# Kernel optimization log

Measured on AMD Instinct MI355X. Metric: run time of the kernel, lower is better.

## Reference

```python
import jax, jax.numpy as jnp
import numpy as np

TEMP = 0.07  # softmax temperature T


def _l2norm(x, axis=1, eps=1e-12):
    return x / jnp.clip(jnp.linalg.norm(x, axis=axis, keepdims=True), eps, None)


def setup_inputs() -> dict:
    key = jax.random.key(0)
    k1, k2, k3, k4 = jax.random.split(key, 4)
    B, K, D = 256, 8192, 128
    q = jax.random.normal(k1, (B, D), dtype=jnp.float32)
    ba_queue = _l2norm(jax.random.normal(k2, (K, D), dtype=jnp.float32))
    nonba_queue = _l2norm(jax.random.normal(k3, (K, D), dtype=jnp.float32))
    targets = jax.random.randint(k4, (B,), 0, 2, dtype=jnp.int64)
    return {"q": q, "ba_queue": ba_queue, "nonba_queue": nonba_queue, "targets": targets}


def reference(q, ba_queue, nonba_queue, targets):
    K = ba_queue.shape[0]
    # encoder output is L2-normalized; queues are detached buffers
    qn = _l2norm(q, axis=1)
    all_feature = jnp.concatenate([qn, ba_queue, nonba_queue], axis=0)  # [N, D]
    all_label = jnp.concatenate([
        targets.astype(jnp.int32),
        jnp.ones((K,), dtype=jnp.int32),
        jnp.zeros((K,), dtype=jnp.int32),
    ])  # [N]
    N = all_feature.shape[0]

    # [N, N] similarity logits
    sim = jnp.matmul(all_feature, all_feature.T) / TEMP
    logits = sim - jax.lax.stop_gradient(jnp.max(sim, axis=1, keepdims=True))

    # positive mask (same label), excluding self
    mask = (all_label[:, None] == all_label[None, :]).astype(jnp.float32)
    logits_mask = 1.0 - jnp.eye(N, dtype=jnp.float32)
    mask = mask * logits_mask

    exp_logits = jnp.exp(logits) * logits_mask
    log_prob = logits - jnp.log(jnp.sum(exp_logits, axis=1, keepdims=True))
    mean_log_prob_pos = jnp.sum(mask * log_prob, axis=1) / jnp.sum(mask, axis=1)
    return -jnp.mean(mean_log_prob_pos)
```

## Files before the change

kernel.cpp:

```cpp
#include <hip/hip_runtime.h>
#include <hip/hip_bf16.h>
#include <stdint.h>

#define TEMPERATURE 0.07f
#define SC 20.6099312f

constexpr int NQ = 256;
constexpr int KQ = 8192;
constexpr int D  = 128;
constexpr int N  = NQ + 2 * KQ;
constexpr int CS = 26;
constexpr int CS2 = CS * 2;
constexpr int BN = 128;
constexpr int RBM = N / 128;
constexpr int RBF = N / 256;
constexpr int PB = 520;
constexpr int LB = 16;

typedef float f32x16 __attribute__((ext_vector_type(16)));
typedef int   i32x4  __attribute__((ext_vector_type(4)));
typedef int   i32x8  __attribute__((ext_vector_type(8)));

constexpr size_t OFF_F32  = 0;
constexpr size_t OFF_8    = OFF_F32  + (size_t)NQ * D * 4;
constexpr size_t OFF_8S   = OFF_8    + (size_t)N * D;
constexpr size_t OFF_PART = OFF_8S   + (size_t)N * D;
constexpr size_t OFF_LP   = OFF_PART + (size_t)CS2 * N * 4;
constexpr size_t OFF_LP2  = OFF_LP   + (size_t)PB * 256 * 4;
constexpr size_t OFF_BSUM = OFF_LP2  + (size_t)LB * 256 * 4;

#define MFMA8(a, b, c) __builtin_amdgcn_mfma_scale_f32_32x32x64_f8f6f4( \
    (a), (b), (c), 0, 0, 0, 0x7f7f7f7f, 0, 0x7f7f7f7f)

__global__ __launch_bounds__(256) void k_prep(const float* __restrict__ q,
                                              const float* __restrict__ ba,
                                              const float* __restrict__ nb,
                                              const long long* __restrict__ tgt,
                                              float* __restrict__ ff,
                                              unsigned char* __restrict__ fb8,
                                              unsigned char* __restrict__ fb8s,
                                              float* __restrict__ lp) {
    __shared__ float red[4][2][128];
    int wid = threadIdx.x >> 6, lane = threadIdx.x & 63;
    int rbase = blockIdx.x * 32 + wid * 8;
    float s0x = 0.f, s0y = 0.f, s1x = 0.f, s1y = 0.f;
    #pragma unroll
    for (int i = 0; i < 8; ++i) {
        int r = rbase + i;
        const float* src = (r < NQ) ? (q + (size_t)r * D)
                         : (r < NQ + KQ) ? (ba + (size_t)(r - NQ) * D)
                         : (nb + (size_t)(r - NQ - KQ) * D);
        float2 v = *(const float2*)(src + lane * 2);
        float a = v.x, b = v.y;
        int lab;
        if (r < NQ) {
            float ss = a * a + b * b;
            #pragma unroll
            for (int m = 1; m < 64; m <<= 1) ss += __shfl_xor(ss, m);
            float scale = 1.0f / fmaxf(sqrtf(ss), 1e-12f);
            a *= scale; b *= scale;
            lab = (int)tgt[r];
            *(float2*)(ff + (size_t)r * D + lane * 2) = make_float2(a, b);
        } else {
            lab = (r < NQ + KQ) ? 1 : 0;
        }
        int w8  = __builtin_amdgcn_cvt_pk_fp8_f32(a, b, 0, false);
        int w8s = __builtin_amdgcn_cvt_pk_fp8_f32(a * SC, b * SC, 0, false);
        *(unsigned short*)(fb8  + (size_t)r * D + lane * 2) = (unsigned short)w8;
        *(unsigned short*)(fb8s + (size_t)r * D + lane * 2) = (unsigned short)w8s;
        if (lab) { s1x += a; s1y += b; } else { s0x += a; s0y += b; }
    }
    red[wid][0][lane * 2]     = s0x;
    red[wid][0][lane * 2 + 1] = s0y;
    red[wid][1][lane * 2]     = s1x;
    red[wid][1][lane * 2 + 1] = s1y;
    __syncthreads();
    int lab2 = threadIdx.x >> 7, d = threadIdx.x & 127;
    float s = red[0][lab2][d] + red[1][lab2][d] + red[2][lab2][d] + red[3][lab2][d];
    lp[(size_t)blockIdx.x * 256 + lab2 * 128 + d] = s;
}

__global__ __launch_bounds__(256) void k_lsum(const float* __restrict__ lp,
                                              float* __restrict__ lp2) {
    int t = threadIdx.x;
    int b0 = blockIdx.x * 33, b1 = min(b0 + 33, PB);
    float s[4] = {0.f, 0.f, 0.f, 0.f};
    for (int b = b0; b < b1; b += 4) {
        #pragma unroll
        for (int j = 0; j < 4; ++j)
            if (b + j < b1) s[j] += lp[(size_t)(b + j) * 256 + t];
    }
    lp2[(size_t)blockIdx.x * 256 + t] = (s[0] + s[1]) + (s[2] + s[3]);
}

__global__ __launch_bounds__(256, 4) void k_main(const unsigned char* __restrict__ fb8,
                                                 const unsigned char* __restrict__ fb8s,
                                                 float* __restrict__ part) {
    __shared__ __align__(16) unsigned char lds[2][BN * 128];
    const int bid = blockIdx.x;
    const int rb = bid / CS, cs = bid % CS;
    const int tid = threadIdx.x;
    const int lane = tid & 63;
    const int wid  = tid >> 6;
    const int wr = wid >> 1, wc = wid & 1;
    const int l31 = lane & 31, lhi = lane >> 5;
    const int rw = rb * 128 + wr * 64;

    int soff[4];
    #pragma unroll
    for (int i = 0; i < 4; ++i) {
        int flat = i * 256 + tid;
        int line = flat >> 4, p = flat & 15;
        int pl = p ^ (line & 15);
        soff[i] = (2 * line + (pl >> 3)) * 128 + (pl & 7) * 16;
    }

#define STAGE(T, B) { \
    const unsigned char* base_ = fb8 + ((size_t)(cs + (T) * CS)) * (BN * 128); \
    _Pragma("unroll") \
    for (int i_ = 0; i_ < 4; ++i_) \
        __builtin_amdgcn_global_load_lds( \
            (const __attribute__((address_space(1))) unsigned int*)(base_ + soff[i_]), \
            (__attribute__((address_space(3))) unsigned int*)(&lds[B][(i_ * 256 + tid) * 16]), \
            16, 0, 0); }

#define SYNC() { asm volatile("s_waitcnt vmcnt(0)" ::: "memory"); __builtin_amdgcn_s_barrier(); }

    i32x8 rf[2][2];
    #pragma unroll
    for (int rs = 0; rs < 2; ++rs)
        #pragma unroll
        for (int s = 0; s < 2; ++s)
            rf[rs][s] = *(const i32x8*)(fb8s + (size_t)(rw + rs * 32 + l31) * D + s * 64 + lhi * 32);

    f32x16 z16;
    #pragma unroll
    for (int e = 0; e < 16; ++e) z16[e] = 0.f;

    float2 ps2[2] = {{0.f, 0.f}, {0.f, 0.f}};

    STAGE(0, 0) SYNC()

    #pragma unroll 1
    for (int t = 0; t < 5; ++t) {
        if (t + 1 < 5) STAGE(t + 1, (t & 1) ^ 1)
        const unsigned char* buf = &lds[t & 1][0];

        f32x16 acc[2][2];
        __builtin_amdgcn_s_setprio(1);
        #pragma unroll
        for (int s = 0; s < 2; ++s) {
            #pragma unroll
            for (int cc = 0; cc < 2; ++cc) {
                int crow = wc * 64 + cc * 32 + l31;
                int line = crow >> 1;
                int pb = ((crow & 1) << 3) + s * 4 + lhi * 2;
                const unsigned char* lb = buf + line * 256;
                i32x4 lo = *(const i32x4*)(lb + ((pb    ) ^ (line & 15)) * 16);
                i32x4 hi = *(const i32x4*)(lb + ((pb + 1) ^ (line & 15)) * 16);
                i32x8 a = {lo[0], lo[1], lo[2], lo[3], hi[0], hi[1], hi[2], hi[3]};
                acc[cc][0] = MFMA8(a, rf[0][s], (s == 0) ? z16 : acc[cc][0]);
                acc[cc][1] = MFMA8(a, rf[1][s], (s == 0) ? z16 : acc[cc][1]);
            }
        }
        __builtin_amdgcn_s_setprio(0);

        #pragma unroll
        for (int cc = 0; cc < 2; ++cc)
            #pragma unroll
            for (int rs = 0; rs < 2; ++rs) {
                float2 p = {0.f, 0.f};
                #pragma unroll
                for (int g = 0; g < 8; ++g) {
                    p.x += __builtin_amdgcn_exp2f(acc[cc][rs][2 * g]);
                    p.y += __builtin_amdgcn_exp2f(acc[cc][rs][2 * g + 1]);
                }
                ps2[rs].x += p.x; ps2[rs].y += p.y;
            }

        SYNC()
    }

    float rsum[2] = {ps2[0].x + ps2[0].y, ps2[1].x + ps2[1].y};
    rsum[0] += __shfl_xor(rsum[0], 32);
    rsum[1] += __shfl_xor(rsum[1], 32);
    if (lane < 32) {
        float* dst = part + (size_t)(cs * 2 + wc) * N + rw + lane;
        dst[0]  = rsum[0];
        dst[32] = rsum[1];
    }
#undef STAGE
#undef SYNC
}

__global__ __launch_bounds__(256) void k_rowfin(const float* __restrict__ part,
                                                const float* __restrict__ ff,
                                                const float* __restrict__ ba,
                                                const float* __restrict__ nb,
                                                const float* __restrict__ lp2,
                                                const long long* __restrict__ tgt,
                                                float* __restrict__ bsum) {
    __shared__ float sS[256];
    __shared__ float red[256];
    __shared__ int scnt[2];
    {
        float s[4] = {0.f, 0.f, 0.f, 0.f};
        #pragma unroll
        for (int b = 0; b < LB; b += 4) {
            #pragma unroll
            for (int j = 0; j < 4; ++j)
                s[j] += lp2[(size_t)(b + j) * 256 + threadIdx.x];
        }
        sS[threadIdx.x] = (s[0] + s[1]) + (s[2] + s[3]);
        if (threadIdx.x < 64) {
            int c = 0;
            #pragma unroll
            for (int i = 0; i < 4; ++i) c += (int)tgt[threadIdx.x + 64 * i];
            #pragma unroll
            for (int m = 1; m < 64; m <<= 1) c += __shfl_xor(c, m);
            if (threadIdx.x == 0) { scnt[0] = (NQ - c) + KQ; scnt[1] = c + KQ; }
        }
    }
    __syncthreads();
    int r = blockIdx.x * 256 + threadIdx.x;
    float se = 0.f;
    #pragma unroll 4
    for (int c = 0; c < CS2; ++c) se += part[(size_t)c * N + r];
    int lab = (r < NQ) ? (int)tgt[r] : ((r < NQ + KQ) ? 1 : 0);
    const float* fsrc = (r < NQ) ? (ff + (size_t)r * D)
                      : (r < NQ + KQ) ? (ba + (size_t)(r - NQ) * D)
                      : (nb + (size_t)(r - NQ - KQ) * D);
    const float4* frow = (const float4*)fsrc;
    const float4* srow = (const float4*)(sS + lab * 128);
    float dS = 0.f, dd = 0.f;
    #pragma unroll
    for (int i = 0; i < 32; ++i) {
        float4 f = frow[i];
        float4 s = srow[i];
        dS += f.x * s.x + f.y * s.y + f.z * s.z + f.w * s.w;
        int wa  = __builtin_amdgcn_cvt_pk_fp8_f32(f.x, f.y, 0, false);
        int wb  = __builtin_amdgcn_cvt_pk_fp8_f32(f.z, f.w, 0, false);
        int wsa = __builtin_amdgcn_cvt_pk_fp8_f32(f.x * SC, f.y * SC, 0, false);
        int wsb = __builtin_amdgcn_cvt_pk_fp8_f32(f.z * SC, f.w * SC, 0, false);
        dd += __builtin_amdgcn_cvt_f32_fp8(wa, 0) * __builtin_amdgcn_cvt_f32_fp8(wsa, 0)
            + __builtin_amdgcn_cvt_f32_fp8(wa, 1) * __builtin_amdgcn_cvt_f32_fp8(wsa, 1)
            + __builtin_amdgcn_cvt_f32_fp8(wb, 0) * __builtin_amdgcn_cvt_f32_fp8(wsb, 0)
            + __builtin_amdgcn_cvt_f32_fp8(wb, 1) * __builtin_amdgcn_cvt_f32_fp8(wsb, 1);
    }
    se -= __builtin_amdgcn_exp2f(dd);
    float lse = logf(se);
    float P = (float)(scnt[lab] - 1);
    float mlpp = (dS - 1.0f) / (TEMPERATURE * P) - lse;
    red[threadIdx.x] = mlpp;
    __syncthreads();
    for (int s2 = 128; s2 > 0; s2 >>= 1) {
        if (threadIdx.x < s2) red[threadIdx.x] += red[threadIdx.x + s2];
        __syncthreads();
    }
    if (threadIdx.x == 0) bsum[blockIdx.x] = red[0];
}

__global__ __launch_bounds__(64) void k_final(const float* __restrict__ bsum,
                                              float* __restrict__ out) {
    float s = bsum[threadIdx.x];
    if (threadIdx.x == 0) s += bsum[64];
    #pragma unroll
    for (int m = 1; m < 64; m <<= 1) s += __shfl_xor(s, m);
    if (threadIdx.x == 0) out[0] = -s / (float)N;
}

extern "C" void kernel_launch(void* const* d_in, const int* in_sizes, int n_in,
                              void* d_out, int out_size, void* d_ws, size_t ws_size,
                              hipStream_t stream) {
    const float* q       = (const float*)d_in[0];
    const float* ba      = (const float*)d_in[1];
    const float* nb      = (const float*)d_in[2];
    const long long* tgt = (const long long*)d_in[3];
    char* ws = (char*)d_ws;
    float*         ff   = (float*)(ws + OFF_F32);
    unsigned char* fb8  = (unsigned char*)(ws + OFF_8);
    unsigned char* fb8s = (unsigned char*)(ws + OFF_8S);
    float*         part = (float*)(ws + OFF_PART);
    float*         lp   = (float*)(ws + OFF_LP);
    float*         lp2  = (float*)(ws + OFF_LP2);
    float*         bsum = (float*)(ws + OFF_BSUM);

    k_prep  <<<PB,       256, 0, stream>>>(q, ba, nb, tgt, ff, fb8, fb8s, lp);
    k_lsum  <<<LB,       256, 0, stream>>>(lp, lp2);
    k_main  <<<RBM * CS, 256, 0, stream>>>(fb8, fb8s, part);
    k_rowfin<<<RBF,      256, 0, stream>>>(part, ff, ba, nb, lp2, tgt, bsum);
    k_final <<<1,         64, 0, stream>>>(bsum, (float*)d_out);
}
```

Baseline: 82.18 us.

## Fuse all stages into one cooperative persistent kernel with grid syncs

Wraps the five kernels (prep, label sum, fp8 MFMA similarity pass, row finalize, final reduce) as device functions and runs them in one cooperative kernel. The grid is sized to the occupancy limit (at most 4 blocks per CU times 256 CUs), and stages are separated by grid.sync. The aim is to remove the per-kernel launch gaps between stages. In exchange, grid-wide barriers are added, the grid-stride loops may balance work worse than one block per tile, and the fused kernel's register use may be constrained by the shared launch bounds. Falls back to the separate launches if the cooperative launch fails.

```diff
diff --git a/kernel.cpp b/kernel.cpp
--- a/kernel.cpp
+++ b/kernel.cpp
@@ -1,6 +1,9 @@
 #include <hip/hip_runtime.h>
+#include <hip/hip_cooperative_groups.h>
 #include <hip/hip_bf16.h>
 #include <stdint.h>
+
+namespace cg = cooperative_groups;
 
 #define TEMPERATURE 0.07f
 #define SC 20.6099312f
@@ -13,6 +16,7 @@
 constexpr int CS2 = CS * 2;
 constexpr int BN = 128;
 constexpr int RBM = N / 128;
+constexpr int NJOB = RBM * CS;
 constexpr int RBF = N / 256;
 constexpr int PB = 520;
 constexpr int LB = 16;
@@ -32,17 +36,19 @@
 #define MFMA8(a, b, c) __builtin_amdgcn_mfma_scale_f32_32x32x64_f8f6f4( \
     (a), (b), (c), 0, 0, 0, 0x7f7f7f7f, 0, 0x7f7f7f7f)
 
-__global__ __launch_bounds__(256) void k_prep(const float* __restrict__ q,
-                                              const float* __restrict__ ba,
-                                              const float* __restrict__ nb,
-                                              const long long* __restrict__ tgt,
-                                              float* __restrict__ ff,
-                                              unsigned char* __restrict__ fb8,
-                                              unsigned char* __restrict__ fb8s,
-                                              float* __restrict__ lp) {
+
+__device__ __forceinline__ void prep_body(int bb,
+                                          const float* __restrict__ q,
+                                          const float* __restrict__ ba,
+                                          const float* __restrict__ nb,
+                                          const long long* __restrict__ tgt,
+                                          float* __restrict__ ff,
+                                          unsigned char* __restrict__ fb8,
+                                          unsigned char* __restrict__ fb8s,
+                                          float* __restrict__ lp) {
     __shared__ float red[4][2][128];
     int wid = threadIdx.x >> 6, lane = threadIdx.x & 63;
-    int rbase = blockIdx.x * 32 + wid * 8;
+    int rbase = bb * 32 + wid * 8;
     float s0x = 0.f, s0y = 0.f, s1x = 0.f, s1y = 0.f;
     #pragma unroll
     for (int i = 0; i < 8; ++i) {
@@ -77,27 +83,29 @@
     __syncthreads();
     int lab2 = threadIdx.x >> 7, d = threadIdx.x & 127;
     float s = red[0][lab2][d] + red[1][lab2][d] + red[2][lab2][d] + red[3][lab2][d];
-    lp[(size_t)blockIdx.x * 256 + lab2 * 128 + d] = s;
-}
-
-__global__ __launch_bounds__(256) void k_lsum(const float* __restrict__ lp,
-                                              float* __restrict__ lp2) {
+    lp[(size_t)bb * 256 + lab2 * 128 + d] = s;
+    __syncthreads();
+}
+
+__device__ __forceinline__ void lsum_body(int bb,
+                                          const float* __restrict__ lp,
+                                          float* __restrict__ lp2) {
     int t = threadIdx.x;
-    int b0 = blockIdx.x * 33, b1 = min(b0 + 33, PB);
+    int b0 = bb * 33, b1 = (b0 + 33 < PB) ? b0 + 33 : PB;
     float s[4] = {0.f, 0.f, 0.f, 0.f};
     for (int b = b0; b < b1; b += 4) {
         #pragma unroll
         for (int j = 0; j < 4; ++j)
             if (b + j < b1) s[j] += lp[(size_t)(b + j) * 256 + t];
     }
-    lp2[(size_t)blockIdx.x * 256 + t] = (s[0] + s[1]) + (s[2] + s[3]);
-}
-
-__global__ __launch_bounds__(256, 4) void k_main(const unsigned char* __restrict__ fb8,
-                                                 const unsigned char* __restrict__ fb8s,
-                                                 float* __restrict__ part) {
+    lp2[(size_t)bb * 256 + t] = (s[0] + s[1]) + (s[2] + s[3]);
+}
+
+__device__ __forceinline__ void main_body(int bid,
+                                          const unsigned char* __restrict__ fb8,
+                                          const unsigned char* __restrict__ fb8s,
+                                          float* __restrict__ part) {
     __shared__ __align__(16) unsigned char lds[2][BN * 128];
-    const int bid = blockIdx.x;
     const int rb = bid / CS, cs = bid % CS;
     const int tid = threadIdx.x;
     const int lane = tid & 63;
@@ -193,13 +201,14 @@
 #undef SYNC
 }
 
-__global__ __launch_bounds__(256) void k_rowfin(const float* __restrict__ part,
-                                                const float* __restrict__ ff,
-                                                const float* __restrict__ ba,
-                                                const float* __restrict__ nb,
-                                                const float* __restrict__ lp2,
-                                                const long long* __restrict__ tgt,
-                                                float* __restrict__ bsum) {
+__device__ __forceinline__ void rowfin_body(int bb,
+                                            const float* __restrict__ part,
+                                            const float* __restrict__ ff,
+                                            const float* __restrict__ ba,
+                                            const float* __restrict__ nb,
+                                            const float* __restrict__ lp2,
+                                            const long long* __restrict__ tgt,
+                                            float* __restrict__ bsum) {
     __shared__ float sS[256];
     __shared__ float red[256];
     __shared__ int scnt[2];
@@ -222,7 +231,7 @@
         }
     }
     __syncthreads();
-    int r = blockIdx.x * 256 + threadIdx.x;
+    int r = bb * 256 + threadIdx.x;
     float se = 0.f;
     #pragma unroll 4
     for (int c = 0; c < CS2; ++c) se += part[(size_t)c * N + r];
@@ -257,25 +266,74 @@
         if (threadIdx.x < s2) red[threadIdx.x] += red[threadIdx.x + s2];
         __syncthreads();
     }
-    if (threadIdx.x == 0) bsum[blockIdx.x] = red[0];
-}
-
-__global__ __launch_bounds__(64) void k_final(const float* __restrict__ bsum,
-                                              float* __restrict__ out) {
-    float s = bsum[threadIdx.x];
-    if (threadIdx.x == 0) s += bsum[64];
-    #pragma unroll
-    for (int m = 1; m < 64; m <<= 1) s += __shfl_xor(s, m);
-    if (threadIdx.x == 0) out[0] = -s / (float)N;
+    if (threadIdx.x == 0) bsum[bb] = red[0];
+    __syncthreads();
+}
+
+__device__ __forceinline__ void final_body(const float* __restrict__ bsum,
+                                           float* __restrict__ out) {
+    if (threadIdx.x < 64) {
+        float s = bsum[threadIdx.x];
+        if (threadIdx.x == 0) s += bsum[64];
+        #pragma unroll
+        for (int m = 1; m < 64; m <<= 1) s += __shfl_xor(s, m);
+        if (threadIdx.x == 0) out[0] = -s / (float)N;
+    }
+}
+
+__global__ __launch_bounds__(256, 4) void k_mega(const float* q, const float* ba,
+                                                 const float* nb, const long long* tgt,
+                                                 float* ff, unsigned char* fb8,
+                                                 unsigned char* fb8s, float* lp,
+                                                 float* lp2, float* part,
+                                                 float* bsum, float* out) {
+    cg::grid_group grid = cg::this_grid();
+    for (int b = blockIdx.x; b < PB; b += gridDim.x)
+        prep_body(b, q, ba, nb, tgt, ff, fb8, fb8s, lp);
+    grid.sync();
+    for (int b = blockIdx.x; b < LB; b += gridDim.x)
+        lsum_body(b, lp, lp2);
+    grid.sync();
+    for (int j = blockIdx.x; j < NJOB; j += gridDim.x)
+        main_body(j, fb8, fb8s, part);
+    grid.sync();
+    for (int b = blockIdx.x; b < RBF; b += gridDim.x)
+        rowfin_body(b, part, ff, ba, nb, lp2, tgt, bsum);
+    grid.sync();
+    if (blockIdx.x == 0) final_body(bsum, out);
+}
+
+__global__ __launch_bounds__(256) void k_prep_k(const float* q, const float* ba,
+                                                const float* nb, const long long* tgt,
+                                                float* ff, unsigned char* fb8,
+                                                unsigned char* fb8s, float* lp) {
+    prep_body(blockIdx.x, q, ba, nb, tgt, ff, fb8, fb8s, lp);
+}
+__global__ __launch_bounds__(256) void k_lsum_k(const float* lp, float* lp2) {
+    lsum_body(blockIdx.x, lp, lp2);
+}
+__global__ __launch_bounds__(256, 4) void k_main_k(const unsigned char* fb8,
+                                                   const unsigned char* fb8s,
+                                                   float* part) {
+    main_body(blockIdx.x, fb8, fb8s, part);
+}
+__global__ __launch_bounds__(256) void k_rowfin_k(const float* part, const float* ff,
+                                                  const float* ba, const float* nb,
+                                                  const float* lp2, const long long* tgt,
+                                                  float* bsum) {
+    rowfin_body(blockIdx.x, part, ff, ba, nb, lp2, tgt, bsum);
+}
+__global__ __launch_bounds__(64) void k_final_k(const float* bsum, float* out) {
+    final_body(bsum, out);
 }
 
 extern "C" void kernel_launch(void* const* d_in, const int* in_sizes, int n_in,
                               void* d_out, int out_size, void* d_ws, size_t ws_size,
                               hipStream_t stream) {
-    const float* q       = (const float*)d_in[0];
-    const float* ba      = (const float*)d_in[1];
-    const float* nb      = (const float*)d_in[2];
-    const long long* tgt = (const long long*)d_in[3];
+    const float* q        = (const float*)d_in[0];
+    const float* ba       = (const float*)d_in[1];
+    const float* nbq      = (const float*)d_in[2];
+    const long long* tgt  = (const long long*)d_in[3];
     char* ws = (char*)d_ws;
     float*         ff   = (float*)(ws + OFF_F32);
     unsigned char* fb8  = (unsigned char*)(ws + OFF_8);
@@ -284,10 +342,26 @@
     float*         lp   = (float*)(ws + OFF_LP);
     float*         lp2  = (float*)(ws + OFF_LP2);
     float*         bsum = (float*)(ws + OFF_BSUM);
-
-    k_prep  <<<PB,       256, 0, stream>>>(q, ba, nb, tgt, ff, fb8, fb8s, lp);
-    k_lsum  <<<LB,       256, 0, stream>>>(lp, lp2);
-    k_main  <<<RBM * CS, 256, 0, stream>>>(fb8, fb8s, part);
-    k_rowfin<<<RBF,      256, 0, stream>>>(part, ff, ba, nb, lp2, tgt, bsum);
-    k_final <<<1,         64, 0, stream>>>(bsum, (float*)d_out);
-}
+    float*         outp = (float*)d_out;
+
+    int maxb = 0;
+    hipError_t qe = hipOccupancyMaxActiveBlocksPerMultiprocessor(
+        &maxb, (const void*)k_mega, 256, 0);
+    bool coop = (qe == hipSuccess && maxb >= 1);
+    if (coop) {
+        int nblk = maxb;
+        if (nblk > 4) nblk = 4;
+        unsigned int grid = (unsigned int)nblk * 256u;
+        void* args[] = {(void*)&q, (void*)&ba, (void*)&nbq, (void*)&tgt,
+                        (void*)&ff, (void*)&fb8, (void*)&fb8s, (void*)&lp,
+                        (void*)&lp2, (void*)&part, (void*)&bsum, (void*)&outp};
+        hipError_t le = hipLaunchCooperativeKernel((void*)k_mega, dim3(grid),
+                                                   dim3(256), args, 0, stream);
+        if (le == hipSuccess) return;
+    }
+    k_prep_k  <<<PB,   256, 0, stream>>>(q, ba, nbq, tgt, ff, fb8, fb8s, lp);
+    k_lsum_k  <<<LB,   256, 0, stream>>>(lp, lp2);
+    k_main_k  <<<NJOB, 256, 0, stream>>>(fb8, fb8s, part);
+    k_rowfin_k<<<RBF,  256, 0, stream>>>(part, ff, ba, nbq, lp2, tgt, bsum);
+    k_final_k <<<1,     64, 0, stream>>>(bsum, outp);
+}
```

Measured after the change: 323.8 us. 294% more time.
